# Optimization experiments

Hardware: AMD Instinct MI355X
Metric: run time of the kernel (lower is better)

Reference implementation:

```python
import jax, jax.numpy as jnp
import numpy as np

G, NPG = 2048, 512          # glimpses, points per glimpse
N0 = G * NPG                # 1,048,576 input points
CPG, CPG2 = 128, 32         # clusters per glimpse at level1/level2
M1, M2 = G * CPG, G * CPG2  # 262144, 65536


def _seg_mean_np(x, ids, m):
    cnt = np.bincount(ids, minlength=m).astype(np.float32)
    out = np.stack([np.bincount(ids, weights=x[:, d], minlength=m) for d in range(x.shape[1])], axis=1)
    return (out / np.maximum(cnt, 1.0)[:, None]).astype(np.float32)


def setup_inputs() -> dict:
    key = jax.random.key(0)
    ks = jax.random.split(key, 16)
    rng = np.random.default_rng(0)
    pos_np = (rng.random((N0, 3)) * 4.0).astype(np.float32)
    # voxel_mean_pool level 0: each point -> a cluster within its glimpse
    g_of_pt = np.arange(N0) // NPG
    out_index0 = (g_of_pt * CPG + rng.integers(0, CPG, N0)).astype(np.int64)
    pos1_np = _seg_mean_np(pos_np, out_index0, M1)
    g_of_c1 = np.arange(M1) // CPG
    out_index1 = (g_of_c1 * CPG2 + rng.integers(0, CPG2, M1)).astype(np.int64)
    pos2_np = _seg_mean_np(pos1_np, out_index1, M2)
    out_index2 = (np.arange(M2) // CPG2).astype(np.int64)  # glimpse id per level-2 point

    def w(k, shp, s=0.05):
        return jax.random.normal(k, shp, dtype=jnp.float32) * s

    return {
        "rgb": jax.random.normal(ks[0], (N0, 1), dtype=jnp.float32),
        "pos": jnp.asarray(pos_np), "pos1": jnp.asarray(pos1_np), "pos2": jnp.asarray(pos2_np),
        "out_index0": jnp.asarray(out_index0), "out_index1": jnp.asarray(out_index1),
        "out_index2": jnp.asarray(out_index2),
        "eps": jax.random.normal(ks[1], (G, 128), dtype=jnp.float32),
        # conv1: local (c_in=1 + 3 -> 16), global (16 -> 32)
        "W1l": w(ks[2], (4, 16)), "b1l": jnp.zeros(16), "W1g": w(ks[3], (16, 32)), "b1g": jnp.zeros(32),
        # conv2: (32+3 -> 64), (64 -> 128)
        "W2l": w(ks[4], (35, 64)), "b2l": jnp.zeros(64), "W2g": w(ks[5], (64, 128)), "b2g": jnp.zeros(128),
        # conv3: (128+3 -> 128), (128 -> 256)
        "W3l": w(ks[6], (131, 128)), "b3l": jnp.zeros(128), "W3g": w(ks[7], (128, 256)), "b3g": jnp.zeros(256),
        "Wlin": w(ks[8], (256, 256)), "blin": jnp.zeros(256),
    }


def _point_conv(x_in, pos_in, pos_out, out_index, Wl, bl, Wg, bg):
    # gather relative position of each input point w.r.t. its output center
    rel = pos_in - pos_out[out_index]                      # [E,3]
    h = jax.nn.celu(jnp.concatenate([x_in, rel], -1) @ Wl + bl)  # per-edge MLP
    m = pos_out.shape[0]
    cnt = jax.ops.segment_sum(jnp.ones((h.shape[0],), h.dtype), out_index, num_segments=m)
    agg = jax.ops.segment_sum(h, out_index, num_segments=m) / jnp.maximum(cnt, 1.0)[:, None]
    return agg @ Wg + bg


def reference(rgb, pos, pos1, pos2, out_index0, out_index1, out_index2, eps,
              W1l, b1l, W1g, b1g, W2l, b2l, W2g, b2g, W3l, b3l, W3g, b3g, Wlin, blin):
    f = rgb  # ar=False path: feature = rgb
    f = jax.nn.celu(_point_conv(f, pos, pos1, out_index0, W1l, b1l, W1g, b1g))   # [M1,32]
    f = jax.nn.celu(_point_conv(f, pos1, pos2, out_index1, W2l, b2l, W2g, b2g))  # [M2,128]
    centers = jnp.zeros((G, 3), f.dtype)  # pos_sample = zeros_like(glimpse__center)
    f = jax.nn.celu(_point_conv(f, pos2, centers, out_index2, W3l, b3l, W3g, b3g))  # [G,256]
    out = f @ Wlin + blin
    mu, sg = jnp.split(out, 2, axis=1)
    sigma = jax.nn.softplus(sg)  # to_sigma
    z = mu + sigma * eps         # Normal.rsample
    z_what, z_mask = jnp.split(z, 2, axis=1)
    return z_what, z_mask, mu, sigma, f
```

## Files before the change

### kernel.cpp

```cpp
#include <hip/hip_runtime.h>
#include <hip/hip_bf16.h>
#include <cstddef>

#define G_   2048
#define NPG_ 512
#define CPG_ 128
#define CPG2_ 32

#define OFF_ZW 0
#define OFF_ZM (G_*64)
#define OFF_MU (2*G_*64)
#define OFF_SG (2*G_*64 + G_*128)
#define OFF_F  (2*G_*64 + 2*G_*128)

typedef __attribute__((ext_vector_type(8))) short bf16x8;
typedef __attribute__((ext_vector_type(4))) float f32x4;
typedef _Float16 f16x2 __attribute__((ext_vector_type(2)));

__device__ __forceinline__ float celu_f(float x)     { return x > 0.f ? x : __expf(x) - 1.f; }
__device__ __forceinline__ float softplus_f(float x) { return fmaxf(x, 0.f) + __logf(1.f + __expf(-fabsf(x))); }
__device__ __forceinline__ unsigned short f2bf(float x) {
    unsigned u = __float_as_uint(x);
    u += 0x7FFFu + ((u >> 16) & 1u);
    return (unsigned short)(u >> 16);
}
__device__ __forceinline__ unsigned pack2(float a, float b) {
    unsigned ua = __float_as_uint(a); ua += 0x7FFFu + ((ua >> 16) & 1u);
    unsigned ub = __float_as_uint(b); ub += 0x7FFFu + ((ub >> 16) & 1u);
    return (ua >> 16) | (ub & 0xFFFF0000u);
}
__device__ __forceinline__ bf16x8 ldb8(const unsigned short* p) {
    union { uint2 u[2]; bf16x8 v; } x;
    x.u[0] = *(const uint2*)p;
    x.u[1] = *(const uint2*)(p + 4);
    return x.v;
}

__global__ void k_prep(const float* __restrict__ W2l, const float* __restrict__ W2g,
                       const float* __restrict__ W3l, const float* __restrict__ W3g,
                       const float* __restrict__ Wlin, const float* __restrict__ W1g,
                       unsigned short* __restrict__ w2lT, unsigned short* __restrict__ w2gT,
                       unsigned short* __restrict__ w3lT, unsigned short* __restrict__ w3gT,
                       unsigned short* __restrict__ wlinT, unsigned short* __restrict__ w1gT)
{
    const int tid = blockIdx.x*256 + threadIdx.x, stride = gridDim.x*256;
    for (int i = tid; i < 64*64; i += stride) {
        const int ch = i >> 6, k = i & 63;
        w2lT[i] = f2bf(k < 35 ? W2l[k*64 + ch] : 0.f);
    }
    for (int i = tid; i < 128*64; i += stride) {
        const int ch = i >> 6, k = i & 63;
        w2gT[i] = f2bf(W2g[k*128 + ch]);
    }
    for (int i = tid; i < 128*160; i += stride) {
        const int ch = i / 160, k = i % 160;
        w3lT[i] = f2bf(k < 131 ? W3l[k*128 + ch] : 0.f);
    }
    for (int i = tid; i < 256*128; i += stride) {
        const int ch = i >> 7, k = i & 127;
        w3gT[i] = f2bf(W3g[k*256 + ch]);
    }
    for (int i = tid; i < 256*256; i += stride) {
        const int ch = i >> 8, k = i & 255;
        wlinT[i] = f2bf(Wlin[k*256 + ch]);
    }
    for (int i = tid; i < 32*40; i += stride) {
        const int ch = i / 40, k = i % 40;
        w1gT[i] = f2bf(k < 16 ? W1g[k*32 + ch] : 0.f);
    }
}

__global__ __launch_bounds__(256, 6) void k_fused(
    const float* __restrict__ rgb, const float* __restrict__ pos, const float* __restrict__ pos1,
    const float* __restrict__ pos2, const int* __restrict__ idx0, const int* __restrict__ idx1,
    const float* __restrict__ W1l, const float* __restrict__ b1l,
    const unsigned short* __restrict__ w1gT, const float* __restrict__ b1g,
    const unsigned short* __restrict__ w2lT, const float* __restrict__ b2l,
    const unsigned short* __restrict__ w2gT, const float* __restrict__ b2g,
    const unsigned short* __restrict__ w3lT, const float* __restrict__ b3l,
    unsigned short* __restrict__ aggws)
{
    const int g = blockIdx.x, t = threadIdx.x;
    const int lane = t & 63, wv = t >> 6;
    const int lr = lane & 15, quad = lane >> 4;

    __shared__ __align__(16) unsigned char smem[27008];
    uint4* const hp4 = (uint4*)smem;
    unsigned short* const aggT  = (unsigned short*)(smem + 16384);
    unsigned short* const xs16  = (unsigned short*)smem;
    unsigned short* const HT    = (unsigned short*)smem;
    unsigned short* const xs3   = (unsigned short*)smem;
    int* const cnt  = (int*)(smem + 25600);
    int* const ctr  = (int*)(smem + 26112);
    int* const cnti = (int*)(smem + 26624);
    int* const wtot = (int*)(smem + 26752);
    unsigned short* const sT   = (unsigned short*)(smem + 18432);
    unsigned short* const agg2 = (unsigned short*)(smem + 18432);
    float* const red  = (float*)(smem + 18432);
    float* const invc = (float*)(smem + 26880);

    if (t < CPG_)  cnt[t]  = 0;
    if (t < CPG2_) cnti[t] = 0;
    int slc_r = 0;
    float relx = 0.f, rely = 0.f, relz = 0.f;
    if (t < CPG_) {
        const int c2 = idx1[g*CPG_ + t];
        slc_r = c2 - g*CPG2_;
        relx = pos1[(g*CPG_ + t)*3 + 0] - pos2[c2*3 + 0];
        rely = pos1[(g*CPG_ + t)*3 + 1] - pos2[c2*3 + 1];
        relz = pos1[(g*CPG_ + t)*3 + 2] - pos2[c2*3 + 2];
    }
    for (int i = t; i < 128*8; i += 256) {
        const int r = i >> 3, j = i & 7;
        ((unsigned*)aggT)[r*18 + 8 + j] = 0u;
    }
    __syncthreads();

    float px0[2], prx[2], pry[2], prz[2];
    int plc[2];
    #pragma unroll
    for (int r = 0; r < 2; r++) {
        const int lp = r*256 + t;
        const int p  = g*NPG_ + lp;
        const int c  = idx0[p];
        plc[r] = c - g*CPG_;
        px0[r] = rgb[p];
        prx[r] = pos[p*3+0] - pos1[c*3+0];
        pry[r] = pos[p*3+1] - pos1[c*3+1];
        prz[r] = pos[p*3+2] - pos1[c*3+2];
        atomicAdd(&cnt[plc[r]], 1);
    }
    if (t < CPG_) atomicAdd(&cnti[slc_r], 1);
    __syncthreads();

    if (t < CPG_) {
        int val = cnt[t];
        const int ln = t & 63;
        #pragma unroll
        for (int d = 1; d < 64; d <<= 1) {
            const int v = __shfl_up(val, d, 64);
            if (ln >= d) val += v;
        }
        ctr[t] = val - cnt[t];
        if (t == 63) *wtot = val;
    }
    if (t < CPG2_) invc[t] = 1.f / fmaxf((float)cnti[t], 1.f);
    __syncthreads();

    const int wtotv = *wtot;

    #pragma unroll
    for (int r = 0; r < 2; r++) {
        unsigned hpk[8];
        #pragma unroll
        for (int j = 0; j < 16; j += 2) {
            const float h0 = celu_f(b1l[j]   + px0[r]*W1l[j]   + prx[r]*W1l[16+j]
                                              + pry[r]*W1l[32+j]   + prz[r]*W1l[48+j]);
            const float h1 = celu_f(b1l[j+1] + px0[r]*W1l[j+1] + prx[r]*W1l[16+j+1]
                                              + pry[r]*W1l[32+j+1] + prz[r]*W1l[48+j+1]);
            union { f16x2 h; unsigned u; } pk;
            pk.h[0] = (_Float16)h0;
            pk.h[1] = (_Float16)h1;
            hpk[j >> 1] = pk.u;
        }
        const int slot = atomicAdd(&ctr[plc[r]], 1) + (plc[r] >= 64 ? wtotv : 0);
        uint4 q0, q1;
        q0.x = hpk[0]; q0.y = hpk[1]; q0.z = hpk[2]; q0.w = hpk[3];
        q1.x = hpk[4]; q1.y = hpk[5]; q1.z = hpk[6]; q1.w = hpk[7];
        hp4[slot]       = q0;
        hp4[512 + slot] = q1;
    }
    __syncthreads();

    const bf16x8 w1g_b0 = *(const bf16x8*)&w1gT[lr*40 + quad*8];
    const bf16x8 w1g_b1 = *(const bf16x8*)&w1gT[(16 + lr)*40 + quad*8];
    const float  b1g_0 = b1g[lr], b1g_1 = b1g[16 + lr];

    {
        const int c = t >> 1, half = t & 1;
        const int n = cnt[c];
        const int base = ctr[c] - n + (c >= 64 ? wtotv : 0);
        const int n0 = (n + 1) >> 1;
        const int sI = base + (half ? n0 : 0);
        const int eI = base + (half ? n  : n0);
        f16x2 acc[8];
        #pragma unroll
        for (int j = 0; j < 8; j++) { union { unsigned u; f16x2 h; } z; z.u = 0u; acc[j] = z.h; }
        for (int i = sI; i < eI; i++) {
            const uint4 a = hp4[i];
            const uint4 b = hp4[512 + i];
            union { unsigned u; f16x2 h; } w;
            w.u = a.x; acc[0] += w.h;  w.u = a.y; acc[1] += w.h;
            w.u = a.z; acc[2] += w.h;  w.u = a.w; acc[3] += w.h;
            w.u = b.x; acc[4] += w.h;  w.u = b.y; acc[5] += w.h;
            w.u = b.z; acc[6] += w.h;  w.u = b.w; acc[7] += w.h;
        }
        #pragma unroll
        for (int j = 0; j < 8; j++) {
            union { unsigned u; f16x2 h; } s, o;
            s.h = acc[j];
            o.u = __shfl_xor(s.u, 1);
            acc[j] += o.h;
        }
        const float inv = 1.f / fmaxf((float)n, 1.f);
        const int ch0 = half * 8, j0 = half * 4;
        float v[8];
        #pragma unroll
        for (int k = 0; k < 4; k++) {
            v[2*k]   = (float)acc[j0+k][0] * inv;
            v[2*k+1] = (float)acc[j0+k][1] * inv;
        }
        uint2 q0, q1;
        q0.x = pack2(v[0], v[1]); q0.y = pack2(v[2], v[3]);
        q1.x = pack2(v[4], v[5]); q1.y = pack2(v[6], v[7]);
        *(uint2*)&aggT[c*36 + ch0]     = q0;
        *(uint2*)&aggT[c*36 + ch0 + 4] = q1;
    }
    __syncthreads();

    f32x4 c1[2][2];
    {
        c1[0][0] = (f32x4){b1g_0, b1g_0, b1g_0, b1g_0};
        c1[0][1] = c1[0][0];
        c1[1][0] = (f32x4){b1g_1, b1g_1, b1g_1, b1g_1};
        c1[1][1] = c1[1][0];
        #pragma unroll
        for (int mt = 0; mt < 2; mt++) {
            const bf16x8 a = ldb8(&aggT[((2*wv + mt)*16 + lr)*36 + quad*8]);
            c1[0][mt] = __builtin_amdgcn_mfma_f32_16x16x32_bf16(a, w1g_b0, c1[0][mt], 0, 0, 0);
            c1[1][mt] = __builtin_amdgcn_mfma_f32_16x16x32_bf16(a, w1g_b1, c1[1][mt], 0, 0, 0);
        }
    }
    __syncthreads();

    {
        const uint4 z4 = {0u, 0u, 0u, 0u};
        for (int i = t; i < 528; i += 256) ((uint4*)sT)[i] = z4;
        for (int i = t; i < 128*5; i += 256) {
            const int r = i / 5, c = 35 + (i - r*5);
            xs16[r*72 + c] = 0;
        }
        for (int i = t; i < 128*3; i += 256) {
            const int r = i / 3, c4 = i - r*3;
            *(uint4*)&xs16[r*72 + 40 + c4*8] = z4;
        }
    }
    #pragma unroll
    for (int nt = 0; nt < 2; nt++)
    #pragma unroll
    for (int mt = 0; mt < 2; mt++)
    #pragma unroll
    for (int r = 0; r < 4; r++) {
        const int cl = (2*wv + mt)*16 + quad*4 + r;
        xs16[cl*72 + nt*16 + lr] = f2bf(celu_f(c1[nt][mt][r]));
    }
    if (t < CPG_) {
        xs16[t*72 + 32] = f2bf(relx);
        xs16[t*72 + 33] = f2bf(rely);
        xs16[t*72 + 34] = f2bf(relz);
    }
    __syncthreads();

    if (t < CPG_) sT[slc_r*132 + t] = 0x3F80;
    float hv[8][4];
    {
        const int chn = wv*16 + lr;
        const bf16x8 bw0 = *(const bf16x8*)&w2lT[chn*64 + quad*8];
        const bf16x8 bw1 = *(const bf16x8*)&w2lT[chn*64 + 32 + quad*8];
        const float bias = b2l[chn];
        #pragma unroll
        for (int m = 0; m < 8; m++) {
            f32x4 acc = (f32x4){bias, bias, bias, bias};
            const bf16x8 a0 = *(const bf16x8*)&xs16[(m*16 + lr)*72 + quad*8];
            const bf16x8 a1 = *(const bf16x8*)&xs16[(m*16 + lr)*72 + 32 + quad*8];
            acc = __builtin_amdgcn_mfma_f32_16x16x32_bf16(a0, bw0, acc, 0, 0, 0);
            acc = __builtin_amdgcn_mfma_f32_16x16x32_bf16(a1, bw1, acc, 0, 0, 0);
            #pragma unroll
            for (int r = 0; r < 4; r++) hv[m][r] = celu_f(acc[r]);
        }
    }
    __syncthreads();

    {
        const int chn = wv*16 + lr;
        #pragma unroll
        for (int m = 0; m < 8; m++) {
            uint2 p;
            p.x = pack2(hv[m][0], hv[m][1]);
            p.y = pack2(hv[m][2], hv[m][3]);
            *(uint2*)&HT[chn*136 + m*16 + quad*4] = p;
        }
    }
    __syncthreads();

    float aggv[2][4];
    {
        const int ch = wv*16 + lr;
        f32x4 acc[2];
        acc[0] = (f32x4){0.f, 0.f, 0.f, 0.f};
        acc[1] = (f32x4){0.f, 0.f, 0.f, 0.f};
        #pragma unroll
        for (int ks = 0; ks < 4; ks++) {
            const bf16x8 b = *(const bf16x8*)&HT[ch*136 + ks*32 + quad*8];
            #pragma unroll
            for (int mt = 0; mt < 2; mt++) {
                const bf16x8 a = ldb8(&sT[(mt*16 + lr)*132 + ks*32 + quad*8]);
                acc[mt] = __builtin_amdgcn_mfma_f32_16x16x32_bf16(a, b, acc[mt], 0, 0, 0);
            }
        }
        #pragma unroll
        for (int mt = 0; mt < 2; mt++)
        #pragma unroll
        for (int r = 0; r < 4; r++)
            aggv[mt][r] = acc[mt][r] * invc[mt*16 + quad*4 + r];
    }
    __syncthreads();

    {
        const int ch = wv*16 + lr;
        #pragma unroll
        for (int mt = 0; mt < 2; mt++)
        #pragma unroll
        for (int r = 0; r < 4; r++)
            agg2[(mt*16 + quad*4 + r)*72 + ch] = f2bf(aggv[mt][r]);
    }
    if (t < CPG2_) {
        #pragma unroll
        for (int d = 0; d < 3; d++)
            xs3[t*168 + 128 + d] = f2bf(pos2[(g*CPG2_ + t)*3 + d]);
    }
    {
        const uint4 z4 = {0u, 0u, 0u, 0u};
        for (int i = t; i < 32*5; i += 256) {
            const int r = i / 5, c = 131 + (i - r*5);
            xs3[r*168 + c] = 0;
        }
        for (int i = t; i < 32*3; i += 256) {
            const int r = i / 3, c4 = i - r*3;
            *(uint4*)&xs3[r*168 + 136 + c4*8] = z4;
        }
    }
    __syncthreads();

    {
        f32x4 acc2[2][2];
        int   chn2[2];
        bf16x8 bw[2][2];
        #pragma unroll
        for (int nt = 0; nt < 2; nt++) {
            chn2[nt] = (wv + nt*4)*16 + lr;
            const float bias = b2g[chn2[nt]];
            #pragma unroll
            for (int mt = 0; mt < 2; mt++) acc2[nt][mt] = (f32x4){bias, bias, bias, bias};
            bw[nt][0] = *(const bf16x8*)&w2gT[chn2[nt]*64 + quad*8];
            bw[nt][1] = *(const bf16x8*)&w2gT[chn2[nt]*64 + 32 + quad*8];
        }
        #pragma unroll
        for (int ks = 0; ks < 2; ks++) {
            #pragma unroll
            for (int mt = 0; mt < 2; mt++) {
                const bf16x8 a = *(const bf16x8*)&agg2[(mt*16 + lr)*72 + ks*32 + quad*8];
                acc2[0][mt] = __builtin_amdgcn_mfma_f32_16x16x32_bf16(a, bw[0][ks], acc2[0][mt], 0, 0, 0);
                acc2[1][mt] = __builtin_amdgcn_mfma_f32_16x16x32_bf16(a, bw[1][ks], acc2[1][mt], 0, 0, 0);
            }
        }
        #pragma unroll
        for (int nt = 0; nt < 2; nt++)
        #pragma unroll
        for (int mt = 0; mt < 2; mt++)
        #pragma unroll
        for (int r = 0; r < 4; r++) {
            const int row = mt*16 + quad*4 + r;
            xs3[row*168 + chn2[nt]] = f2bf(celu_f(acc2[nt][mt][r]));
        }
    }
    __syncthreads();

    {
        f32x4 acc[2][2];
        int chn[2];
        #pragma unroll
        for (int nt = 0; nt < 2; nt++) {
            chn[nt] = (wv + nt*4)*16 + lr;
            const float bias = b3l[chn[nt]];
            #pragma unroll
            for (int mt = 0; mt < 2; mt++) acc[nt][mt] = (f32x4){bias, bias, bias, bias};
        }
        #pragma unroll
        for (int ks = 0; ks < 5; ks++) {
            const bf16x8 b0 = *(const bf16x8*)&w3lT[chn[0]*160 + ks*32 + quad*8];
            const bf16x8 b1 = *(const bf16x8*)&w3lT[chn[1]*160 + ks*32 + quad*8];
            #pragma unroll
            for (int mt = 0; mt < 2; mt++) {
                const bf16x8 a = *(const bf16x8*)&xs3[(mt*16 + lr)*168 + ks*32 + quad*8];
                acc[0][mt] = __builtin_amdgcn_mfma_f32_16x16x32_bf16(a, b0, acc[0][mt], 0, 0, 0);
                acc[1][mt] = __builtin_amdgcn_mfma_f32_16x16x32_bf16(a, b1, acc[1][mt], 0, 0, 0);
            }
        }
        #pragma unroll
        for (int nt = 0; nt < 2; nt++)
        #pragma unroll
        for (int mt = 0; mt < 2; mt++) {
            const float p = celu_f(acc[nt][mt][0]) + celu_f(acc[nt][mt][1])
                          + celu_f(acc[nt][mt][2]) + celu_f(acc[nt][mt][3]);
            red[chn[nt]*9 + mt*4 + quad] = p;
        }
    }
    __syncthreads();

    if (t < 128) {
        const float* rp = &red[t*9];
        float a = 0.f;
        #pragma unroll
        for (int p = 0; p < 8; p++) a += rp[p];
        aggws[(size_t)g*128 + t] = f2bf(a * (1.f/32.f));
    }
}

__global__ __launch_bounds__(256) void k_head(
    const unsigned short* __restrict__ aggws,
    const unsigned short* __restrict__ w3gT, const float* __restrict__ b3g,
    const unsigned short* __restrict__ wlinT, const float* __restrict__ blin,
    const float* __restrict__ eps, float* __restrict__ out)
{
    const int g0 = blockIdx.x * 16, t = threadIdx.x;
    const int lane = t & 63, wv = t >> 6;
    const int lr = lane & 15, quad = lane >> 4;
    __shared__ __align__(16) unsigned short aggB[16*136];
    __shared__ __align__(16) unsigned short f3B[16*264];

    {
        const int row = t >> 4, col8 = (t & 15) * 8;
        const uint4 v = ((const uint4*)aggws)[(size_t)g0*16 + t];
        *(uint4*)&aggB[row*136 + col8] = v;
    }
    __syncthreads();

    {
        f32x4 c3[4];
        int ch3[4];
        #pragma unroll
        for (int nt = 0; nt < 4; nt++) {
            ch3[nt] = (wv + nt*4)*16 + lr;
            const float bias = b3g[ch3[nt]];
            c3[nt] = (f32x4){bias, bias, bias, bias};
        }
        #pragma unroll
        for (int ks = 0; ks < 4; ks++) {
            const bf16x8 a = *(const bf16x8*)&aggB[lr*136 + ks*32 + quad*8];
            #pragma unroll
            for (int nt = 0; nt < 4; nt++) {
                const bf16x8 b = *(const bf16x8*)&w3gT[ch3[nt]*128 + ks*32 + quad*8];
                c3[nt] = __builtin_amdgcn_mfma_f32_16x16x32_bf16(a, b, c3[nt], 0, 0, 0);
            }
        }
        #pragma unroll
        for (int nt = 0; nt < 4; nt++)
        #pragma unroll
        for (int r = 0; r < 4; r++) {
            const int row = quad*4 + r;
            const float v = celu_f(c3[nt][r]);
            out[OFF_F + (size_t)(g0 + row)*256 + ch3[nt]] = v;
            f3B[row*264 + ch3[nt]] = f2bf(v);
        }
    }
    __syncthreads();

    {
        f32x4 cl[4];
        int ch4[4];
        #pragma unroll
        for (int nt = 0; nt < 4; nt++) {
            ch4[nt] = (wv + nt*4)*16 + lr;
            const float bias = blin[ch4[nt]];
            cl[nt] = (f32x4){bias, bias, bias, bias};
        }
        #pragma unroll
        for (int ks = 0; ks < 8; ks++) {
            const bf16x8 a = *(const bf16x8*)&f3B[lr*264 + ks*32 + quad*8];
            #pragma unroll
            for (int nt = 0; nt < 4; nt++) {
                const bf16x8 b = *(const bf16x8*)&wlinT[ch4[nt]*256 + ks*32 + quad*8];
                cl[nt] = __builtin_amdgcn_mfma_f32_16x16x32_bf16(a, b, cl[nt], 0, 0, 0);
            }
        }
        #pragma unroll
        for (int nt = 0; nt < 2; nt++)
        #pragma unroll
        for (int r = 0; r < 4; r++) {
            const int row = quad*4 + r;
            const int g = g0 + row;
            const int ch = ch4[nt];
            const float mu    = cl[nt][r];
            const float sigma = softplus_f(cl[nt + 2][r]);
            const float z     = mu + sigma * eps[(size_t)g*128 + ch];
            out[OFF_MU + (size_t)g*128 + ch] = mu;
            out[OFF_SG + (size_t)g*128 + ch] = sigma;
            if (nt == 0) out[OFF_ZW + (size_t)g*64 + ch] = z;
            else         out[OFF_ZM + (size_t)g*64 + (ch - 64)] = z;
        }
    }
}

extern "C" void kernel_launch(void* const* d_in, const int* in_sizes, int n_in,
                              void* d_out, int out_size, void* d_ws, size_t ws_size,
                              hipStream_t stream)
{
    const float* rgb  = (const float*)d_in[0];
    const float* pos  = (const float*)d_in[1];
    const float* pos1 = (const float*)d_in[2];
    const float* pos2 = (const float*)d_in[3];
    const int*   idx0 = (const int*)d_in[4];
    const int*   idx1 = (const int*)d_in[5];
    const float* eps  = (const float*)d_in[7];
    const float* W1l = (const float*)d_in[8],  *b1l = (const float*)d_in[9];
    const float* W1g = (const float*)d_in[10], *b1g = (const float*)d_in[11];
    const float* W2l = (const float*)d_in[12], *b2l = (const float*)d_in[13];
    const float* W2g = (const float*)d_in[14], *b2g = (const float*)d_in[15];
    const float* W3l = (const float*)d_in[16], *b3l = (const float*)d_in[17];
    const float* W3g = (const float*)d_in[18], *b3g = (const float*)d_in[19];
    const float* Wlin = (const float*)d_in[20], *blin = (const float*)d_in[21];

    unsigned short* w2lT  = (unsigned short*)d_ws;
    unsigned short* w2gT  = w2lT + 64*64;
    unsigned short* w3lT  = w2gT + 128*64;
    unsigned short* w3gT  = w3lT + 128*160;
    unsigned short* wlinT = w3gT + 256*128;
    unsigned short* w1gT  = wlinT + 256*256;
    unsigned short* aggws = w1gT + 32*40;
    float* outp = (float*)d_out;

    k_prep <<<64,    256, 0, stream>>>(W2l, W2g, W3l, W3g, Wlin, W1g,
                                       w2lT, w2gT, w3lT, w3gT, wlinT, w1gT);
    k_fused<<<G_,    256, 0, stream>>>(rgb, pos, pos1, pos2, idx0, idx1,
                                       W1l, b1l, w1gT, b1g,
                                       w2lT, b2l, w2gT, b2g, w3lT, b3l, aggws);
    k_head <<<G_/16, 256, 0, stream>>>(aggws, w3gT, b3g, wlinT, blin, eps, outp);
}
```

Before: 156.7 us.

## Process two glimpses per block in fused point-conv kernel

Each block of the fused kernel now handles two glimpses instead of one, doubling shared memory and halving the grid, and lowering the occupancy hint from 6 to 3 blocks per SM. Per-block weight fragments such as w2l, w2g and the b3l biases are loaded once and reused for both glimpses, and the level-2 and level-3 stages are interleaved across glimpses, which lets some barriers cover two steps. This is meant to amortize weight loads, barriers and per-block launch overhead. The cost is fewer resident blocks and more serialized work per block, which may hide latency less well.

```diff
diff --git a/kernel.cpp b/kernel.cpp
--- a/kernel.cpp
+++ b/kernel.cpp
@@ -70,7 +70,7 @@
     }
 }
 
-__global__ __launch_bounds__(256, 6) void k_fused(
+__global__ __launch_bounds__(256, 3) void k_fused(
     const float* __restrict__ rgb, const float* __restrict__ pos, const float* __restrict__ pos1,
     const float* __restrict__ pos2, const int* __restrict__ idx0, const int* __restrict__ idx1,
     const float* __restrict__ W1l, const float* __restrict__ b1l,
@@ -80,95 +80,104 @@
     const unsigned short* __restrict__ w3lT, const float* __restrict__ b3l,
     unsigned short* __restrict__ aggws)
 {
-    const int g = blockIdx.x, t = threadIdx.x;
+    const int g0 = blockIdx.x * 2, t = threadIdx.x;
     const int lane = t & 63, wv = t >> 6;
     const int lr = lane & 15, quad = lane >> 4;
-
-    __shared__ __align__(16) unsigned char smem[27008];
+    const int myg = t >> 7;
+    const int th  = t & 127;
+
+    __shared__ __align__(16) unsigned char smem[54016];
     uint4* const hp4 = (uint4*)smem;
-    unsigned short* const aggT  = (unsigned short*)(smem + 16384);
-    unsigned short* const xs16  = (unsigned short*)smem;
-    unsigned short* const HT    = (unsigned short*)smem;
-    unsigned short* const xs3   = (unsigned short*)smem;
-    int* const cnt  = (int*)(smem + 25600);
-    int* const ctr  = (int*)(smem + 26112);
-    int* const cnti = (int*)(smem + 26624);
-    int* const wtot = (int*)(smem + 26752);
-    unsigned short* const sT   = (unsigned short*)(smem + 18432);
-    unsigned short* const agg2 = (unsigned short*)(smem + 18432);
-    float* const red  = (float*)(smem + 18432);
-    float* const invc = (float*)(smem + 26880);
-
-    if (t < CPG_)  cnt[t]  = 0;
-    if (t < CPG2_) cnti[t] = 0;
-    int slc_r = 0;
-    float relx = 0.f, rely = 0.f, relz = 0.f;
-    if (t < CPG_) {
-        const int c2 = idx1[g*CPG_ + t];
-        slc_r = c2 - g*CPG2_;
-        relx = pos1[(g*CPG_ + t)*3 + 0] - pos2[c2*3 + 0];
-        rely = pos1[(g*CPG_ + t)*3 + 1] - pos2[c2*3 + 1];
-        relz = pos1[(g*CPG_ + t)*3 + 2] - pos2[c2*3 + 2];
-    }
-    for (int i = t; i < 128*8; i += 256) {
+    unsigned short* const aggT = (unsigned short*)(smem + 32768);
+    int* const cnt  = (int*)(smem + 51200);
+    int* const ctr  = (int*)(smem + 52224);
+    int* const cnti = (int*)(smem + 53248);
+    int* const wtot = (int*)(smem + 53504);
+    unsigned short* const xs16 = (unsigned short*)smem;
+    unsigned short* const sT   = (unsigned short*)(smem + 36864);
+    unsigned short* const HT   = (unsigned short*)smem;
+    unsigned short* const xs3  = (unsigned short*)smem;
+    unsigned short* const agg2 = (unsigned short*)(smem + 36864);
+    float* const red  = (float*)(smem + 36864);
+    float* const invc = (float*)(smem + 53760);
+
+    cnt[t] = 0;
+    if (t < 64) cnti[t] = 0;
+    int slc_r; float relx, rely, relz;
+    {
+        const int gm = g0 + myg;
+        const int c2 = idx1[gm*CPG_ + th];
+        slc_r = c2 - gm*CPG2_;
+        relx = pos1[(gm*CPG_ + th)*3 + 0] - pos2[c2*3 + 0];
+        rely = pos1[(gm*CPG_ + th)*3 + 1] - pos2[c2*3 + 1];
+        relz = pos1[(gm*CPG_ + th)*3 + 2] - pos2[c2*3 + 2];
+    }
+    for (int i = t; i < 256*8; i += 256) {
         const int r = i >> 3, j = i & 7;
         ((unsigned*)aggT)[r*18 + 8 + j] = 0u;
     }
     __syncthreads();
 
-    float px0[2], prx[2], pry[2], prz[2];
-    int plc[2];
+    float px0[2][2], prx[2][2], pry[2][2], prz[2][2];
+    int plc[2][2];
+    #pragma unroll
+    for (int gi = 0; gi < 2; gi++)
     #pragma unroll
     for (int r = 0; r < 2; r++) {
-        const int lp = r*256 + t;
-        const int p  = g*NPG_ + lp;
-        const int c  = idx0[p];
-        plc[r] = c - g*CPG_;
-        px0[r] = rgb[p];
-        prx[r] = pos[p*3+0] - pos1[c*3+0];
-        pry[r] = pos[p*3+1] - pos1[c*3+1];
-        prz[r] = pos[p*3+2] - pos1[c*3+2];
-        atomicAdd(&cnt[plc[r]], 1);
-    }
-    if (t < CPG_) atomicAdd(&cnti[slc_r], 1);
-    __syncthreads();
-
-    if (t < CPG_) {
-        int val = cnt[t];
+        const int p = (g0 + gi)*NPG_ + r*256 + t;
+        const int c = idx0[p];
+        plc[gi][r] = c - (g0 + gi)*CPG_;
+        px0[gi][r] = rgb[p];
+        prx[gi][r] = pos[p*3+0] - pos1[c*3+0];
+        pry[gi][r] = pos[p*3+1] - pos1[c*3+1];
+        prz[gi][r] = pos[p*3+2] - pos1[c*3+2];
+        atomicAdd(&cnt[gi*128 + plc[gi][r]], 1);
+    }
+    atomicAdd(&cnti[myg*32 + slc_r], 1);
+    __syncthreads();
+
+    {
+        const int v0 = cnt[myg*128 + th];
+        int val = v0;
         const int ln = t & 63;
         #pragma unroll
         for (int d = 1; d < 64; d <<= 1) {
             const int v = __shfl_up(val, d, 64);
             if (ln >= d) val += v;
         }
-        ctr[t] = val - cnt[t];
-        if (t == 63) *wtot = val;
-    }
-    if (t < CPG2_) invc[t] = 1.f / fmaxf((float)cnti[t], 1.f);
-    __syncthreads();
-
-    const int wtotv = *wtot;
-
-    #pragma unroll
-    for (int r = 0; r < 2; r++) {
-        unsigned hpk[8];
-        #pragma unroll
-        for (int j = 0; j < 16; j += 2) {
-            const float h0 = celu_f(b1l[j]   + px0[r]*W1l[j]   + prx[r]*W1l[16+j]
-                                              + pry[r]*W1l[32+j]   + prz[r]*W1l[48+j]);
-            const float h1 = celu_f(b1l[j+1] + px0[r]*W1l[j+1] + prx[r]*W1l[16+j+1]
-                                              + pry[r]*W1l[32+j+1] + prz[r]*W1l[48+j+1]);
-            union { f16x2 h; unsigned u; } pk;
-            pk.h[0] = (_Float16)h0;
-            pk.h[1] = (_Float16)h1;
-            hpk[j >> 1] = pk.u;
-        }
-        const int slot = atomicAdd(&ctr[plc[r]], 1) + (plc[r] >= 64 ? wtotv : 0);
-        uint4 q0, q1;
-        q0.x = hpk[0]; q0.y = hpk[1]; q0.z = hpk[2]; q0.w = hpk[3];
-        q1.x = hpk[4]; q1.y = hpk[5]; q1.z = hpk[6]; q1.w = hpk[7];
-        hp4[slot]       = q0;
-        hp4[512 + slot] = q1;
+        ctr[myg*128 + th] = val - v0;
+        if ((t & 127) == 63) wtot[myg] = val;
+    }
+    if (t < 64) invc[t] = 1.f / fmaxf((float)cnti[t], 1.f);
+    __syncthreads();
+
+    const int wt0 = wtot[0], wt1 = wtot[1];
+
+    #pragma unroll
+    for (int gi = 0; gi < 2; gi++) {
+        const int wtg = gi ? wt1 : wt0;
+        #pragma unroll
+        for (int r = 0; r < 2; r++) {
+            unsigned hpk[8];
+            #pragma unroll
+            for (int j = 0; j < 16; j += 2) {
+                const float h0 = celu_f(b1l[j]   + px0[gi][r]*W1l[j]   + prx[gi][r]*W1l[16+j]
+                                                  + pry[gi][r]*W1l[32+j]   + prz[gi][r]*W1l[48+j]);
+                const float h1 = celu_f(b1l[j+1] + px0[gi][r]*W1l[j+1] + prx[gi][r]*W1l[16+j+1]
+                                                  + pry[gi][r]*W1l[32+j+1] + prz[gi][r]*W1l[48+j+1]);
+                union { f16x2 h; unsigned u; } pk;
+                pk.h[0] = (_Float16)h0;
+                pk.h[1] = (_Float16)h1;
+                hpk[j >> 1] = pk.u;
+            }
+            const int pc = plc[gi][r];
+            const int slot = atomicAdd(&ctr[gi*128 + pc], 1) + (pc >= 64 ? wtg : 0);
+            uint4 q0, q1;
+            q0.x = hpk[0]; q0.y = hpk[1]; q0.z = hpk[2]; q0.w = hpk[3];
+            q1.x = hpk[4]; q1.y = hpk[5]; q1.z = hpk[6]; q1.w = hpk[7];
+            hp4[gi*1024 + slot]       = q0;
+            hp4[gi*1024 + 512 + slot] = q1;
+        }
     }
     __syncthreads();
 
@@ -178,130 +187,146 @@
 
     {
         const int c = t >> 1, half = t & 1;
-        const int n = cnt[c];
-        const int base = ctr[c] - n + (c >= 64 ? wtotv : 0);
-        const int n0 = (n + 1) >> 1;
-        const int sI = base + (half ? n0 : 0);
-        const int eI = base + (half ? n  : n0);
-        f16x2 acc[8];
-        #pragma unroll
-        for (int j = 0; j < 8; j++) { union { unsigned u; f16x2 h; } z; z.u = 0u; acc[j] = z.h; }
-        for (int i = sI; i < eI; i++) {
-            const uint4 a = hp4[i];
-            const uint4 b = hp4[512 + i];
-            union { unsigned u; f16x2 h; } w;
-            w.u = a.x; acc[0] += w.h;  w.u = a.y; acc[1] += w.h;
-            w.u = a.z; acc[2] += w.h;  w.u = a.w; acc[3] += w.h;
-            w.u = b.x; acc[4] += w.h;  w.u = b.y; acc[5] += w.h;
-            w.u = b.z; acc[6] += w.h;  w.u = b.w; acc[7] += w.h;
-        }
-        #pragma unroll
-        for (int j = 0; j < 8; j++) {
-            union { unsigned u; f16x2 h; } s, o;
-            s.h = acc[j];
-            o.u = __shfl_xor(s.u, 1);
-            acc[j] += o.h;
-        }
-        const float inv = 1.f / fmaxf((float)n, 1.f);
         const int ch0 = half * 8, j0 = half * 4;
-        float v[8];
-        #pragma unroll
-        for (int k = 0; k < 4; k++) {
-            v[2*k]   = (float)acc[j0+k][0] * inv;
-            v[2*k+1] = (float)acc[j0+k][1] * inv;
-        }
-        uint2 q0, q1;
-        q0.x = pack2(v[0], v[1]); q0.y = pack2(v[2], v[3]);
-        q1.x = pack2(v[4], v[5]); q1.y = pack2(v[6], v[7]);
-        *(uint2*)&aggT[c*36 + ch0]     = q0;
-        *(uint2*)&aggT[c*36 + ch0 + 4] = q1;
-    }
-    __syncthreads();
-
-    f32x4 c1[2][2];
-    {
-        c1[0][0] = (f32x4){b1g_0, b1g_0, b1g_0, b1g_0};
-        c1[0][1] = c1[0][0];
-        c1[1][0] = (f32x4){b1g_1, b1g_1, b1g_1, b1g_1};
-        c1[1][1] = c1[1][0];
+        #pragma unroll
+        for (int gi = 0; gi < 2; gi++) {
+            const int n = cnt[gi*128 + c];
+            const int wtg = gi ? wt1 : wt0;
+            const int base = ctr[gi*128 + c] - n + (c >= 64 ? wtg : 0);
+            const int n0 = (n + 1) >> 1;
+            const int sI = base + (half ? n0 : 0);
+            const int eI = base + (half ? n  : n0);
+            f16x2 acc[8];
+            #pragma unroll
+            for (int j = 0; j < 8; j++) { union { unsigned u; f16x2 h; } z; z.u = 0u; acc[j] = z.h; }
+            for (int i = sI; i < eI; i++) {
+                const uint4 a = hp4[gi*1024 + i];
+                const uint4 b = hp4[gi*1024 + 512 + i];
+                union { unsigned u; f16x2 h; } w;
+                w.u = a.x; acc[0] += w.h;  w.u = a.y; acc[1] += w.h;
+                w.u = a.z; acc[2] += w.h;  w.u = a.w; acc[3] += w.h;
+                w.u = b.x; acc[4] += w.h;  w.u = b.y; acc[5] += w.h;
+                w.u = b.z; acc[6] += w.h;  w.u = b.w; acc[7] += w.h;
+            }
+            #pragma unroll
+            for (int j = 0; j < 8; j++) {
+                union { unsigned u; f16x2 h; } s, o;
+                s.h = acc[j];
+                o.u = __shfl_xor(s.u, 1);
+                acc[j] += o.h;
+            }
+            const float inv = 1.f / fmaxf((float)n, 1.f);
+            float v[8];
+            #pragma unroll
+            for (int k = 0; k < 4; k++) {
+                v[2*k]   = (float)acc[j0+k][0] * inv;
+                v[2*k+1] = (float)acc[j0+k][1] * inv;
+            }
+            uint2 q0, q1;
+            q0.x = pack2(v[0], v[1]); q0.y = pack2(v[2], v[3]);
+            q1.x = pack2(v[4], v[5]); q1.y = pack2(v[6], v[7]);
+            *(uint2*)&aggT[(gi*128 + c)*36 + ch0]     = q0;
+            *(uint2*)&aggT[(gi*128 + c)*36 + ch0 + 4] = q1;
+        }
+    }
+    __syncthreads();
+
+    f32x4 c1[2][2][2];
+    #pragma unroll
+    for (int gi = 0; gi < 2; gi++) {
+        c1[gi][0][0] = (f32x4){b1g_0, b1g_0, b1g_0, b1g_0};
+        c1[gi][0][1] = c1[gi][0][0];
+        c1[gi][1][0] = (f32x4){b1g_1, b1g_1, b1g_1, b1g_1};
+        c1[gi][1][1] = c1[gi][1][0];
         #pragma unroll
         for (int mt = 0; mt < 2; mt++) {
-            const bf16x8 a = ldb8(&aggT[((2*wv + mt)*16 + lr)*36 + quad*8]);
-            c1[0][mt] = __builtin_amdgcn_mfma_f32_16x16x32_bf16(a, w1g_b0, c1[0][mt], 0, 0, 0);
-            c1[1][mt] = __builtin_amdgcn_mfma_f32_16x16x32_bf16(a, w1g_b1, c1[1][mt], 0, 0, 0);
+            const bf16x8 a = ldb8(&aggT[(gi*128 + (2*wv + mt)*16 + lr)*36 + quad*8]);
+            c1[gi][0][mt] = __builtin_amdgcn_mfma_f32_16x16x32_bf16(a, w1g_b0, c1[gi][0][mt], 0, 0, 0);
+            c1[gi][1][mt] = __builtin_amdgcn_mfma_f32_16x16x32_bf16(a, w1g_b1, c1[gi][1][mt], 0, 0, 0);
         }
     }
     __syncthreads();
 
     {
         const uint4 z4 = {0u, 0u, 0u, 0u};
-        for (int i = t; i < 528; i += 256) ((uint4*)sT)[i] = z4;
-        for (int i = t; i < 128*5; i += 256) {
+        for (int i = t; i < 1056; i += 256) ((uint4*)sT)[i] = z4;
+        for (int i = t; i < 256*5; i += 256) {
             const int r = i / 5, c = 35 + (i - r*5);
             xs16[r*72 + c] = 0;
         }
-        for (int i = t; i < 128*3; i += 256) {
+        for (int i = t; i < 256*3; i += 256) {
             const int r = i / 3, c4 = i - r*3;
             *(uint4*)&xs16[r*72 + 40 + c4*8] = z4;
         }
     }
     #pragma unroll
+    for (int gi = 0; gi < 2; gi++)
+    #pragma unroll
     for (int nt = 0; nt < 2; nt++)
     #pragma unroll
     for (int mt = 0; mt < 2; mt++)
     #pragma unroll
     for (int r = 0; r < 4; r++) {
         const int cl = (2*wv + mt)*16 + quad*4 + r;
-        xs16[cl*72 + nt*16 + lr] = f2bf(celu_f(c1[nt][mt][r]));
-    }
-    if (t < CPG_) {
-        xs16[t*72 + 32] = f2bf(relx);
-        xs16[t*72 + 33] = f2bf(rely);
-        xs16[t*72 + 34] = f2bf(relz);
-    }
-    __syncthreads();
-
-    if (t < CPG_) sT[slc_r*132 + t] = 0x3F80;
+        xs16[(gi*128 + cl)*72 + nt*16 + lr] = f2bf(celu_f(c1[gi][nt][mt][r]));
+    }
+    xs16[(myg*128 + th)*72 + 32] = f2bf(relx);
+    xs16[(myg*128 + th)*72 + 33] = f2bf(rely);
+    xs16[(myg*128 + th)*72 + 34] = f2bf(relz);
+    __syncthreads();
+
+    sT[(myg*32 + slc_r)*132 + th] = 0x3F80;
+    const int chn = wv*16 + lr;
+    const bf16x8 bw2l0 = *(const bf16x8*)&w2lT[chn*64 + quad*8];
+    const bf16x8 bw2l1 = *(const bf16x8*)&w2lT[chn*64 + 32 + quad*8];
+    const float  b2lv  = b2l[chn];
     float hv[8][4];
-    {
-        const int chn = wv*16 + lr;
-        const bf16x8 bw0 = *(const bf16x8*)&w2lT[chn*64 + quad*8];
-        const bf16x8 bw1 = *(const bf16x8*)&w2lT[chn*64 + 32 + quad*8];
-        const float bias = b2l[chn];
-        #pragma unroll
-        for (int m = 0; m < 8; m++) {
-            f32x4 acc = (f32x4){bias, bias, bias, bias};
-            const bf16x8 a0 = *(const bf16x8*)&xs16[(m*16 + lr)*72 + quad*8];
-            const bf16x8 a1 = *(const bf16x8*)&xs16[(m*16 + lr)*72 + 32 + quad*8];
-            acc = __builtin_amdgcn_mfma_f32_16x16x32_bf16(a0, bw0, acc, 0, 0, 0);
-            acc = __builtin_amdgcn_mfma_f32_16x16x32_bf16(a1, bw1, acc, 0, 0, 0);
-            #pragma unroll
-            for (int r = 0; r < 4; r++) hv[m][r] = celu_f(acc[r]);
-        }
-    }
-    __syncthreads();
-
-    {
-        const int chn = wv*16 + lr;
-        #pragma unroll
-        for (int m = 0; m < 8; m++) {
-            uint2 p;
-            p.x = pack2(hv[m][0], hv[m][1]);
-            p.y = pack2(hv[m][2], hv[m][3]);
-            *(uint2*)&HT[chn*136 + m*16 + quad*4] = p;
-        }
-    }
-    __syncthreads();
-
+    #pragma unroll
+    for (int m = 0; m < 8; m++) {
+        f32x4 acc = (f32x4){b2lv, b2lv, b2lv, b2lv};
+        const bf16x8 a0 = *(const bf16x8*)&xs16[(m*16 + lr)*72 + quad*8];
+        const bf16x8 a1 = *(const bf16x8*)&xs16[(m*16 + lr)*72 + 32 + quad*8];
+        acc = __builtin_amdgcn_mfma_f32_16x16x32_bf16(a0, bw2l0, acc, 0, 0, 0);
+        acc = __builtin_amdgcn_mfma_f32_16x16x32_bf16(a1, bw2l1, acc, 0, 0, 0);
+        #pragma unroll
+        for (int r = 0; r < 4; r++) hv[m][r] = celu_f(acc[r]);
+    }
+    __syncthreads();
+
+    #pragma unroll
+    for (int m = 0; m < 8; m++) {
+        uint2 p;
+        p.x = pack2(hv[m][0], hv[m][1]);
+        p.y = pack2(hv[m][2], hv[m][3]);
+        *(uint2*)&HT[chn*136 + m*16 + quad*4] = p;
+    }
+    #pragma unroll
+    for (int m = 0; m < 8; m++) {
+        f32x4 acc = (f32x4){b2lv, b2lv, b2lv, b2lv};
+        const bf16x8 a0 = *(const bf16x8*)&xs16[(128 + m*16 + lr)*72 + quad*8];
+        const bf16x8 a1 = *(const bf16x8*)&xs16[(128 + m*16 + lr)*72 + 32 + quad*8];
+        acc = __builtin_amdgcn_mfma_f32_16x16x32_bf16(a0, bw2l0, acc, 0, 0, 0);
+        acc = __builtin_amdgcn_mfma_f32_16x16x32_bf16(a1, bw2l1, acc, 0, 0, 0);
+        #pragma unroll
+        for (int r = 0; r < 4; r++) hv[m][r] = celu_f(acc[r]);
+    }
+    __syncthreads();
+
+    #pragma unroll
+    for (int m = 0; m < 8; m++) {
+        uint2 p;
+        p.x = pack2(hv[m][0], hv[m][1]);
+        p.y = pack2(hv[m][2], hv[m][3]);
+        *(uint2*)&HT[(64 + chn)*136 + m*16 + quad*4] = p;
+    }
     float aggv[2][4];
     {
-        const int ch = wv*16 + lr;
         f32x4 acc[2];
         acc[0] = (f32x4){0.f, 0.f, 0.f, 0.f};
         acc[1] = (f32x4){0.f, 0.f, 0.f, 0.f};
         #pragma unroll
         for (int ks = 0; ks < 4; ks++) {
-            const bf16x8 b = *(const bf16x8*)&HT[ch*136 + ks*32 + quad*8];
+            const bf16x8 b = *(const bf16x8*)&HT[chn*136 + ks*32 + quad*8];
             #pragma unroll
             for (int mt = 0; mt < 2; mt++) {
                 const bf16x8 a = ldb8(&sT[(mt*16 + lr)*132 + ks*32 + quad*8]);
@@ -316,18 +341,15 @@
     }
     __syncthreads();
 
-    {
-        const int ch = wv*16 + lr;
-        #pragma unroll
-        for (int mt = 0; mt < 2; mt++)
-        #pragma unroll
-        for (int r = 0; r < 4; r++)
-            agg2[(mt*16 + quad*4 + r)*72 + ch] = f2bf(aggv[mt][r]);
-    }
+    #pragma unroll
+    for (int mt = 0; mt < 2; mt++)
+    #pragma unroll
+    for (int r = 0; r < 4; r++)
+        agg2[(mt*16 + quad*4 + r)*72 + chn] = f2bf(aggv[mt][r]);
     if (t < CPG2_) {
         #pragma unroll
         for (int d = 0; d < 3; d++)
-            xs3[t*168 + 128 + d] = f2bf(pos2[(g*CPG2_ + t)*3 + d]);
+            xs3[t*168 + 128 + d] = f2bf(pos2[(g0*CPG2_ + t)*3 + d]);
     }
     {
         const uint4 z4 = {0u, 0u, 0u, 0u};
@@ -340,28 +362,71 @@
             *(uint4*)&xs3[r*168 + 136 + c4*8] = z4;
         }
     }
-    __syncthreads();
-
+    {
+        f32x4 acc[2];
+        acc[0] = (f32x4){0.f, 0.f, 0.f, 0.f};
+        acc[1] = (f32x4){0.f, 0.f, 0.f, 0.f};
+        #pragma unroll
+        for (int ks = 0; ks < 4; ks++) {
+            const bf16x8 b = *(const bf16x8*)&HT[(64 + chn)*136 + ks*32 + quad*8];
+            #pragma unroll
+            for (int mt = 0; mt < 2; mt++) {
+                const bf16x8 a = ldb8(&sT[(32 + mt*16 + lr)*132 + ks*32 + quad*8]);
+                acc[mt] = __builtin_amdgcn_mfma_f32_16x16x32_bf16(a, b, acc[mt], 0, 0, 0);
+            }
+        }
+        #pragma unroll
+        for (int mt = 0; mt < 2; mt++)
+        #pragma unroll
+        for (int r = 0; r < 4; r++)
+            aggv[mt][r] = acc[mt][r] * invc[32 + mt*16 + quad*4 + r];
+    }
+    __syncthreads();
+
+    #pragma unroll
+    for (int mt = 0; mt < 2; mt++)
+    #pragma unroll
+    for (int r = 0; r < 4; r++)
+        agg2[(32 + mt*16 + quad*4 + r)*72 + chn] = f2bf(aggv[mt][r]);
+    if (t < CPG2_) {
+        #pragma unroll
+        for (int d = 0; d < 3; d++)
+            xs3[(32 + t)*168 + 128 + d] = f2bf(pos2[((g0 + 1)*CPG2_ + t)*3 + d]);
+    }
+    {
+        const uint4 z4 = {0u, 0u, 0u, 0u};
+        for (int i = t; i < 32*5; i += 256) {
+            const int r = i / 5, c = 131 + (i - r*5);
+            xs3[(32 + r)*168 + c] = 0;
+        }
+        for (int i = t; i < 32*3; i += 256) {
+            const int r = i / 3, c4 = i - r*3;
+            *(uint4*)&xs3[(32 + r)*168 + 136 + c4*8] = z4;
+        }
+    }
+    int chn2[2];
+    bf16x8 bw2g[2][2];
+    float b2gv[2];
+    #pragma unroll
+    for (int nt = 0; nt < 2; nt++) {
+        chn2[nt] = (wv + nt*4)*16 + lr;
+        b2gv[nt] = b2g[chn2[nt]];
+        bw2g[nt][0] = *(const bf16x8*)&w2gT[chn2[nt]*64 + quad*8];
+        bw2g[nt][1] = *(const bf16x8*)&w2gT[chn2[nt]*64 + 32 + quad*8];
+    }
     {
         f32x4 acc2[2][2];
-        int   chn2[2];
-        bf16x8 bw[2][2];
-        #pragma unroll
-        for (int nt = 0; nt < 2; nt++) {
-            chn2[nt] = (wv + nt*4)*16 + lr;
-            const float bias = b2g[chn2[nt]];
-            #pragma unroll
-            for (int mt = 0; mt < 2; mt++) acc2[nt][mt] = (f32x4){bias, bias, bias, bias};
-            bw[nt][0] = *(const bf16x8*)&w2gT[chn2[nt]*64 + quad*8];
-            bw[nt][1] = *(const bf16x8*)&w2gT[chn2[nt]*64 + 32 + quad*8];
-        }
+        #pragma unroll
+        for (int nt = 0; nt < 2; nt++)
+        #pragma unroll
+        for (int mt = 0; mt < 2; mt++) acc2[nt][mt] = (f32x4){b2gv[nt], b2gv[nt], b2gv[nt], b2gv[nt]};
         #pragma unroll
         for (int ks = 0; ks < 2; ks++) {
             #pragma unroll
             for (int mt = 0; mt < 2; mt++) {
                 const bf16x8 a = *(const bf16x8*)&agg2[(mt*16 + lr)*72 + ks*32 + quad*8];
-                acc2[0][mt] = __builtin_amdgcn_mfma_f32_16x16x32_bf16(a, bw[0][ks], acc2[0][mt], 0, 0, 0);
-                acc2[1][mt] = __builtin_amdgcn_mfma_f32_16x16x32_bf16(a, bw[1][ks], acc2[1][mt], 0, 0, 0);
+                acc2[0][mt] = __builtin_amdgcn_mfma_f32_16x16x32_bf16(a, bw2g[0][ks], acc2[0][mt], 0, 0, 0);
+                acc2[1][mt] = __builtin_amdgcn_mfma_f32_16x16x32_bf16(a, bw2g[1][ks], acc2[1][mt], 0, 0, 0);
             }
         }
         #pragma unroll
@@ -377,19 +442,41 @@
     __syncthreads();
 
     {
+        f32x4 acc2[2][2];
+        #pragma unroll
+        for (int nt = 0; nt < 2; nt++)
+        #pragma unroll
+        for (int mt = 0; mt < 2; mt++) acc2[nt][mt] = (f32x4){b2gv[nt], b2gv[nt], b2gv[nt], b2gv[nt]};
+        #pragma unroll
+        for (int ks = 0; ks < 2; ks++) {
+            #pragma unroll
+            for (int mt = 0; mt < 2; mt++) {
+                const bf16x8 a = *(const bf16x8*)&agg2[(32 + mt*16 + lr)*72 + ks*32 + quad*8];
+                acc2[0][mt] = __builtin_amdgcn_mfma_f32_16x16x32_bf16(a, bw2g[0][ks], acc2[0][mt], 0, 0, 0);
+                acc2[1][mt] = __builtin_amdgcn_mfma_f32_16x16x32_bf16(a, bw2g[1][ks], acc2[1][mt], 0, 0, 0);
+            }
+        }
+        #pragma unroll
+        for (int nt = 0; nt < 2; nt++)
+        #pragma unroll
+        for (int mt = 0; mt < 2; mt++)
+        #pragma unroll
+        for (int r = 0; r < 4; r++) {
+            const int row = mt*16 + quad*4 + r;
+            xs3[(32 + row)*168 + chn2[nt]] = f2bf(celu_f(acc2[nt][mt][r]));
+        }
+    }
+    const float b3lv[2] = {b3l[chn2[0]], b3l[chn2[1]]};
+    {
         f32x4 acc[2][2];
-        int chn[2];
-        #pragma unroll
-        for (int nt = 0; nt < 2; nt++) {
-            chn[nt] = (wv + nt*4)*16 + lr;
-            const float bias = b3l[chn[nt]];
-            #pragma unroll
-            for (int mt = 0; mt < 2; mt++) acc[nt][mt] = (f32x4){bias, bias, bias, bias};
-        }
+        #pragma unroll
+        for (int nt = 0; nt < 2; nt++)
+        #pragma unroll
+        for (int mt = 0; mt < 2; mt++) acc[nt][mt] = (f32x4){b3lv[nt], b3lv[nt], b3lv[nt], b3lv[nt]};
         #pragma unroll
         for (int ks = 0; ks < 5; ks++) {
-            const bf16x8 b0 = *(const bf16x8*)&w3lT[chn[0]*160 + ks*32 + quad*8];
-            const bf16x8 b1 = *(const bf16x8*)&w3lT[chn[1]*160 + ks*32 + quad*8];
+            const bf16x8 b0 = *(const bf16x8*)&w3lT[chn2[0]*160 + ks*32 + quad*8];
+            const bf16x8 b1 = *(const bf16x8*)&w3lT[chn2[1]*160 + ks*32 + quad*8];
             #pragma unroll
             for (int mt = 0; mt < 2; mt++) {
                 const bf16x8 a = *(const bf16x8*)&xs3[(mt*16 + lr)*168 + ks*32 + quad*8];
@@ -403,17 +490,52 @@
         for (int mt = 0; mt < 2; mt++) {
             const float p = celu_f(acc[nt][mt][0]) + celu_f(acc[nt][mt][1])
                           + celu_f(acc[nt][mt][2]) + celu_f(acc[nt][mt][3]);
-            red[chn[nt]*9 + mt*4 + quad] = p;
-        }
-    }
-    __syncthreads();
-
+            red[chn2[nt]*9 + mt*4 + quad] = p;
+        }
+    }
+    __syncthreads();
+
+    {
+        f32x4 acc[2][2];
+        #pragma unroll
+        for (int nt = 0; nt < 2; nt++)
+        #pragma unroll
+        for (int mt = 0; mt < 2; mt++) acc[nt][mt] = (f32x4){b3lv[nt], b3lv[nt], b3lv[nt], b3lv[nt]};
+        #pragma unroll
+        for (int ks = 0; ks < 5; ks++) {
+            const bf16x8 b0 = *(const bf16x8*)&w3lT[chn2[0]*160 + ks*32 + quad*8];
+            const bf16x8 b1 = *(const bf16x8*)&w3lT[chn2[1]*160 + ks*32 + quad*8];
+            #pragma unroll
+            for (int mt = 0; mt < 2; mt++) {
+                const bf16x8 a = *(const bf16x8*)&xs3[(32 + mt*16 + lr)*168 + ks*32 + quad*8];
+                acc[0][mt] = __builtin_amdgcn_mfma_f32_16x16x32_bf16(a, b0, acc[0][mt], 0, 0, 0);
+                acc[1][mt] = __builtin_amdgcn_mfma_f32_16x16x32_bf16(a, b1, acc[1][mt], 0, 0, 0);
+            }
+        }
+        #pragma unroll
+        for (int nt = 0; nt < 2; nt++)
+        #pragma unroll
+        for (int mt = 0; mt < 2; mt++) {
+            const float p = celu_f(acc[nt][mt][0]) + celu_f(acc[nt][mt][1])
+                          + celu_f(acc[nt][mt][2]) + celu_f(acc[nt][mt][3]);
+            red[(128 + chn2[nt])*9 + mt*4 + quad] = p;
+        }
+    }
     if (t < 128) {
         const float* rp = &red[t*9];
         float a = 0.f;
         #pragma unroll
         for (int p = 0; p < 8; p++) a += rp[p];
-        aggws[(size_t)g*128 + t] = f2bf(a * (1.f/32.f));
+        aggws[(size_t)g0*128 + t] = f2bf(a * (1.f/32.f));
+    }
+    __syncthreads();
+
+    if (t < 128) {
+        const float* rp = &red[(128 + t)*9];
+        float a = 0.f;
+        #pragma unroll
+        for (int p = 0; p < 8; p++) a += rp[p];
+        aggws[(size_t)(g0 + 1)*128 + t] = f2bf(a * (1.f/32.f));
     }
 }
 
@@ -532,7 +654,7 @@
 
     k_prep <<<64,    256, 0, stream>>>(W2l, W2g, W3l, W3g, Wlin, W1g,
                                        w2lT, w2gT, w3lT, w3gT, wlinT, w1gT);
-    k_fused<<<G_,    256, 0, stream>>>(rgb, pos, pos1, pos2, idx0, idx1,
+    k_fused<<<G_/2,  256, 0, stream>>>(rgb, pos, pos1, pos2, idx0, idx1,
                                        W1l, b1l, w1gT, b1g,
                                        w2lT, b2l, w2gT, b2g, w3lT, b3l, aggws);
     k_head <<<G_/16, 256, 0, stream>>>(aggws, w3gT, b3g, wlinT, blin, eps, outp);
```

Result: no change. 158.8 us (+1.3%).
